# Kernel optimization log

Measured on AMD Instinct MI355X. Metric: run time of the kernel, lower is better.

Reference implementation:

```python
import jax, jax.numpy as jnp
import numpy as np

N_NODES = 20000
N_EDGES = 320000
N_GRAPHS = 200
N_LAYERS = 2
TOWERS = 5
F_IN = 75        # divide_input=False -> each tower sees the full 75-dim input
F_OUT = 15       # out_channels // towers = 75 // 5
EDGE_DIM = 50
POST_IN = (4 * 3 + 1) * F_IN  # 4 aggregators * 3 scalers + self = 975
EPS_STD = 1e-5
EPS_BN = 1e-5


def setup_inputs() -> dict:
    key = jax.random.key(0)
    ks = jax.random.split(key, 16)
    x_idx = jax.random.randint(ks[0], (N_NODES,), 0, 10000)
    edge_index = jax.random.randint(ks[1], (2, N_EDGES), 0, N_NODES)
    edge_attr_idx = jax.random.randint(ks[2], (N_EDGES,), 0, 100)
    batch_idx = jnp.sort(jax.random.randint(ks[3], (N_NODES,), 0, N_GRAPHS))

    def g(k, shp, fan):
        return jax.random.normal(k, shp, jnp.float32) * np.float32(1.0 / np.sqrt(fan))

    inp = dict(
        x_idx=x_idx, edge_index=edge_index, edge_attr_idx=edge_attr_idx, batch_idx=batch_idx,
        node_emb=g(ks[4], (10000, F_IN), 1.0),
        edge_emb=g(ks[5], (100, EDGE_DIM), 1.0),
        W_edge=g(ks[6], (N_LAYERS, EDGE_DIM, F_IN), EDGE_DIM),
        b_edge=jnp.zeros((N_LAYERS, F_IN), jnp.float32),
        W_pre=g(ks[7], (N_LAYERS, TOWERS, 3 * F_IN, F_IN), 3 * F_IN),
        b_pre=jnp.zeros((N_LAYERS, TOWERS, F_IN), jnp.float32),
        W_post=g(ks[8], (N_LAYERS, TOWERS, POST_IN, F_OUT), POST_IN),
        b_post=jnp.zeros((N_LAYERS, TOWERS, F_OUT), jnp.float32),
        W_lin=g(ks[9], (N_LAYERS, F_IN, F_IN), F_IN),
        b_lin=jnp.zeros((N_LAYERS, F_IN), jnp.float32),
        bn_gamma=jnp.ones((N_LAYERS, F_IN), jnp.float32),
        bn_beta=jnp.zeros((N_LAYERS, F_IN), jnp.float32),
        W1=g(ks[10], (75, 50), 75), b1=jnp.zeros((50,), jnp.float32),
        W2=g(ks[11], (50, 25), 50), b2=jnp.zeros((25,), jnp.float32),
        W3=g(ks[12], (25, 1), 25), b3=jnp.zeros((1,), jnp.float32),
    )
    return inp


def reference(x_idx, edge_index, edge_attr_idx, batch_idx,
              node_emb, edge_emb, W_edge, b_edge, W_pre, b_pre,
              W_post, b_post, W_lin, b_lin, bn_gamma, bn_beta,
              W1, b1, W2, b2, W3, b3):
    src, dst = edge_index[0], edge_index[1]  # flow source_to_target: aggregate at dst
    x = node_emb[x_idx]                      # [N, 75]
    e_raw = edge_emb[edge_attr_idx]          # [E, 50]

    # in-degree based scalers (PNA); avg log-degree from this graph's degree histogram
    deg = jax.ops.segment_sum(jnp.ones((N_EDGES,), jnp.float32), dst, num_segments=N_NODES)
    avg_log = jnp.mean(jnp.log(deg + 1.0))
    deg_c = jnp.maximum(deg, 1.0)
    amp = (jnp.log(deg_c + 1.0) / avg_log)[:, None, None]
    att = (avg_log / jnp.log(deg_c + 1.0))[:, None, None]
    has_in = (deg > 0.0)[:, None, None]
    inv_deg = (1.0 / deg_c)[:, None, None]

    for l in range(N_LAYERS):
        # edge encoder (shared across towers)
        e = e_raw @ W_edge[l] + b_edge[l]                            # [E, 75]
        # message: since divide_input=False all towers see the same concat input
        h = jnp.concatenate([x[dst], x[src], e], axis=-1)            # [E, 225]
        m = jnp.einsum('ec,tcf->etf', h, W_pre[l]) + b_pre[l]        # [E, T, 75]
        # multi-aggregator reduction at dst
        mean = jax.ops.segment_sum(m, dst, num_segments=N_NODES) * inv_deg
        mean_sq = jax.ops.segment_sum(m * m, dst, num_segments=N_NODES) * inv_deg
        std = jnp.sqrt(jax.nn.relu(mean_sq - mean * mean) + EPS_STD)
        mn = jnp.where(has_in, jax.ops.segment_min(m, dst, num_segments=N_NODES), 0.0)
        mx = jnp.where(has_in, jax.ops.segment_max(m, dst, num_segments=N_NODES), 0.0)
        aggr = jnp.concatenate([mean, mn, mx, std], axis=-1)         # [N, T, 300]
        # degree scalers: identity, amplification, attenuation
        out = jnp.concatenate([aggr, aggr * amp, aggr * att], axis=-1)  # [N, T, 900]
        # update: concat self features, per-tower post MLP, then shared lin
        xt = jnp.broadcast_to(x[:, None, :], (N_NODES, TOWERS, F_IN))
        h2 = jnp.concatenate([xt, out], axis=-1)                     # [N, T, 975]
        y = jnp.einsum('ntc,tcf->ntf', h2, W_post[l]) + b_post[l]    # [N, T, 15]
        y = y.reshape(N_NODES, TOWERS * F_OUT) @ W_lin[l] + b_lin[l] # [N, 75]
        # BatchNorm (training-mode batch stats, biased variance) + ReLU
        mu = jnp.mean(y, axis=0)
        var = jnp.mean((y - mu) ** 2, axis=0)
        y = (y - mu) * jax.lax.rsqrt(var + EPS_BN) * bn_gamma[l] + bn_beta[l]
        x = jax.nn.relu(y)

    pooled = jax.ops.segment_sum(x, batch_idx, num_segments=N_GRAPHS)  # [G, 75]
    h = jax.nn.relu(pooled @ W1 + b1)
    h = jax.nn.relu(h @ W2 + b2)
    return h @ W3 + b3                                               # [G, 1]
```

## Files before the change

### kernel.cpp

```cpp
#include <hip/hip_runtime.h>
#include <hip/hip_bf16.h>
#include <math.h>

#define NN 20000
#define NE 320000
#define NG 200
#define FI 75
#define NT 5
#define FO 15
#define CH 375
#define PI 975

typedef __attribute__((ext_vector_type(8))) short v8s;
typedef __attribute__((ext_vector_type(4))) float v4f;

__device__ __forceinline__ unsigned short f2bfu(float v) {
  __hip_bfloat16 h = __float2bfloat16(v);
  return *reinterpret_cast<unsigned short*>(&h);
}
__device__ __forceinline__ float uif(unsigned u) { return __uint_as_float(u); }

__global__ __launch_bounds__(256) void k_mega1(
    const int* __restrict__ xidx, const float* __restrict__ emb, float* __restrict__ x,
    const int* __restrict__ dstp, int* __restrict__ deg,
    const float* __restrict__ eemb, const float* __restrict__ W_edge,
    const float* __restrict__ b_edge, float* __restrict__ te,
    const float* __restrict__ W_pre, float* __restrict__ WAs,
    const float* __restrict__ W_post, float* __restrict__ V,
    const float* __restrict__ b_post, const float* __restrict__ W_lin,
    const float* __restrict__ b_lin, float* __restrict__ bc) {
  __shared__ float S[FI * 16];
  int b = blockIdx.x, tid = threadIdx.x;
  if (b < 5860) {
    int i = b * 256 + tid;
    if (i < NN * FI) {
      int n = i / FI, f = i - n * FI;
      x[i] = emb[xidx[n] * FI + f];
    }
  } else if (b < 7110) {
    int e = (b - 5860) * 256 + tid;
    if (e < NE) atomicAdd(&deg[dstp[e]], 1);
  } else if (b < 7310) {
    int la = b - 7110;
    int l = la / 100, a = la - l * 100;
    int f = tid;
    if (f < FI) {
      float acc = b_edge[l * FI + f];
      for (int j = 0; j < 50; ++j)
        acc = fmaf(eemb[a * 50 + j], W_edge[(l * 50 + j) * FI + f], acc);
      te[la * FI + f] = acc;
    }
  } else if (b < 7530) {
    int i = (b - 7310) * 256 + tid;
    if (i < 2 * FI * CH) {
      int c = i % CH;
      int k = (i / CH) % FI;
      int l = i / (CH * FI);
      int t = c / FI, f = c - t * FI;
      WAs[i] = W_pre[((size_t)(l * NT + t) * 225 + FI + k) * FI + f];
    }
  } else if (b < 7560) {
    int bid = b - 7530;
    int g = bid % 3;
    int lt = bid / 3;
    for (int idx = tid; idx < FI * 16; idx += 256) {
      int q = idx >> 4, f = idx & 15;
      float v = 0.f;
      if (f < FO) {
        const float* wb = W_post + (size_t)lt * PI * FO;
        int rowb = FI + g * 300 + q;
        v = wb[rowb * FO + f] + wb[(rowb + FI) * FO + f] + wb[(rowb + 2 * FI) * FO + f];
      }
      S[idx] = v;
    }
    __syncthreads();
    for (int idx = tid; idx < FI * 16; idx += 256) {
      int j = idx >> 4, f = idx & 15;
      float acc = 0.f;
      const float* wr = W_pre + ((size_t)lt * 225 + j) * FI;
      for (int q = 0; q < FI; ++q) acc = fmaf(wr[q], S[q * 16 + f], acc);
      V[((size_t)bid * FI + j) * 16 + f] = acc;
    }
  } else {
    int l = b - 7560;
    int g = tid;
    if (g < FI) {
      float acc = b_lin[l * FI + g];
      for (int j = 0; j < FI; ++j)
        acc = fmaf(b_post[l * FI + j], W_lin[(l * FI + j) * FI + g], acc);
      bc[l * 76 + g] = acc;
    }
  }
}

__global__ __launch_bounds__(1024) void k_mega2(
    const int* __restrict__ deg, int* __restrict__ off, int* __restrict__ cur,
    float* __restrict__ avglog,
    const float* __restrict__ te, const float* __restrict__ W_pre,
    const float* __restrict__ b_pre, unsigned short* __restrict__ tm,
    const float* __restrict__ W_post, const float* __restrict__ V,
    unsigned short* __restrict__ Bp,
    const float* __restrict__ WAs, unsigned short* __restrict__ Bxs,
    const float* __restrict__ W_lin, unsigned short* __restrict__ Blin) {
  __shared__ float red[1024];
  int b = blockIdx.x, t = threadIdx.x;
  if (b == 0) {
    int* wsum = (int*)red;
    int base = t * 20;
    int loc[20];
    int s = 0;
#pragma unroll
    for (int j = 0; j < 20; ++j) {
      int i = base + j;
      int v = (i < NN) ? deg[i] : 0;
      loc[j] = s;
      s += v;
    }
    int lane = t & 63, w = t >> 6;
    int inc = s;
    for (int o = 1; o < 64; o <<= 1) {
      int u = __shfl_up(inc, o, 64);
      if (lane >= o) inc += u;
    }
    if (lane == 63) wsum[w] = inc;
    __syncthreads();
    if (t == 0) {
      int a = 0;
#pragma unroll
      for (int k = 0; k < 16; ++k) { int v = wsum[k]; wsum[k] = a; a += v; }
    }
    __syncthreads();
    int tex = wsum[w] + inc - s;
#pragma unroll
    for (int j = 0; j < 20; ++j) {
      int i = base + j;
      if (i < NN) { int e = tex + loc[j]; off[i] = e; cur[i] = e; }
    }
    if (t == 1023) off[NN] = tex + s;
  } else if (b == 1) {
    float s = 0.f;
    for (int i = t; i < NN; i += 1024) s += logf((float)deg[i] + 1.f);
    red[t] = s;
    __syncthreads();
    for (int o = 512; o > 0; o >>= 1) {
      if (t < o) red[t] += red[t + o];
      __syncthreads();
    }
    if (t == 0) avglog[0] = red[0] / (float)NN;
  } else if (b < 77) {
    int idx = (b - 2) * 1024 + t;
    if (idx < 76800) {
      int la = idx / 384, c = idx - la * 384;
      int l = la / 100;
      float acc = 0.f;
      if (c < CH) {
        int tt = c / FI, f = c - tt * FI;
        acc = b_pre[(l * NT + tt) * FI + f];
        const float* ter = te + la * FI;
        for (int k = 0; k < FI; ++k)
          acc = fmaf(ter[k], W_pre[((size_t)(l * NT + tt) * 225 + 150 + k) * FI + f], acc);
      }
      tm[(size_t)la * 384 + c] = f2bfu(acc);
    }
  } else if (b < 302) {
    int i = (b - 77) * 1024 + t;
    if (i < 230400) {
      int j = i & 7;
      int lane = (i >> 3) & 63;
      int rem = i >> 9;
      int kb = rem % 15; rem /= 15;
      int g = rem % 3; rem /= 3;
      int tt = rem % 5;
      int l = rem / 5;
      int k = kb * 32 + (lane >> 4) * 8 + j;
      int f = lane & 15;
      float w = 0.f;
      if (f < FO) {
        int lt = l * NT + tt;
        if (k < 300) {
          int a = k / 75, ch = k - a * 75;
          w = W_post[((size_t)lt * PI + FI + g * 300 + a * 75 + ch) * FO + f];
        } else if (k >= 320 && k < 395) {
          w = V[(((size_t)(lt * 3 + g)) * FI + (k - 320)) * 16 + f];
        } else if (k >= 395 && k < 470 && g == 0) {
          w = W_post[((size_t)lt * PI + (k - 395)) * FO + f];
        }
      }
      Bp[i] = f2bfu(w);
    }
  } else if (b < 374) {
    int i = (b - 302) * 1024 + t;
    if (i < 73728) {
      int j = i & 7;
      int lane = (i >> 3) & 63;
      int rem = i >> 9;
      int nt = rem % 24; rem /= 24;
      int kb = rem % 3;
      int l = rem / 3;
      int k = kb * 32 + (lane >> 4) * 8 + j;
      int n = nt * 16 + (lane & 15);
      float w = 0.f;
      if (k < FI && n < CH) w = WAs[(size_t)l * FI * CH + k * CH + n];
      Bxs[i] = f2bfu(w);
    }
  } else {
    int i = (b - 374) * 1024 + t;
    if (i < 15360) {
      int j = i & 7;
      int lane = (i >> 3) & 63;
      int rem = i >> 9;
      int nt = rem % 5; rem /= 5;
      int kb = rem % 3;
      int l = rem / 3;
      int k = kb * 32 + (lane >> 4) * 8 + j;
      int f = nt * 16 + (lane & 15);
      float w = 0.f;
      if (k < FI && f < FI) w = W_lin[(size_t)l * FI * FI + k * FI + f];
      Blin[i] = f2bfu(w);
    }
  }
}

__global__ __launch_bounds__(256) void k_mega3(
    const int* __restrict__ srcp, const int* __restrict__ dstp,
    const int* __restrict__ attr, int* __restrict__ cur, int2* __restrict__ csr,
    const int* __restrict__ deg, const float* __restrict__ avglog,
    float* __restrict__ amp, float* __restrict__ att, float* __restrict__ inv) {
  int b = blockIdx.x, t = threadIdx.x;
  if (b < 1250) {
    int e = b * 256 + t;
    if (e < NE) {
      int pos = atomicAdd(&cur[dstp[e]], 1);
      csr[pos] = make_int2(srcp[e], attr[e]);
    }
  } else {
    int i = (b - 1250) * 256 + t;
    if (i < NN) {
      float dc = fmaxf((float)deg[i], 1.f);
      float ld = logf(dc + 1.f);
      float av = avglog[0];
      amp[i] = ld / av;
      att[i] = av / ld;
      inv[i] = 1.f / dc;
    }
  }
}

__global__ __launch_bounds__(256) void k_gemm_xs(const float* __restrict__ x,
                                                 const unsigned short* __restrict__ BxsL,
                                                 unsigned short* __restrict__ xsb,
                                                 const int* __restrict__ deg,
                                                 unsigned short* __restrict__ xh,
                                                 float* __restrict__ bnsum) {
  int tid = threadIdx.x;
  if (blockIdx.y == 1) {
    if (blockIdx.x == 0 && tid < 150) bnsum[tid] = 0.f;
    for (int i = blockIdx.x * 256 + tid; i < NN * 160; i += 625 * 256) {
      int r = i / 160, k = i - r * 160;
      float v = 0.f;
      if (k < FI) v = x[(size_t)r * FI + k] * ((deg[r] > 0) ? 1.f : 0.f);
      else if (k < 150) v = x[(size_t)r * FI + k - FI];
      xh[i] = f2bfu(v);
    }
    return;
  }
  __shared__ unsigned short As[32 * 104];
  __shared__ unsigned short Os[32 * 384];
  int m0 = blockIdx.x * 32;
  for (int i = tid; i < 32 * 104; i += 256) {
    int r = i / 104, k = i - r * 104;
    As[i] = (k < FI) ? f2bfu(x[(size_t)(m0 + r) * FI + k]) : 0;
  }
  __syncthreads();
  int lane = tid & 63, w = tid >> 6;
  int m16 = lane & 15, quad = lane >> 4;
  v4f acc0[6], acc1[6];
#pragma unroll
  for (int nt = 0; nt < 6; ++nt) {
    acc0[nt] = {0.f, 0.f, 0.f, 0.f};
    acc1[nt] = {0.f, 0.f, 0.f, 0.f};
  }
  const unsigned short* arow0 = As + m16 * 104 + quad * 8;
  const unsigned short* arow1 = As + (16 + m16) * 104 + quad * 8;
#pragma unroll
  for (int kb = 0; kb < 3; ++kb) {
    v8s a0 = *(const v8s*)(arow0 + kb * 32);
    v8s a1 = *(const v8s*)(arow1 + kb * 32);
#pragma unroll
    for (int nt = 0; nt < 6; ++nt) {
      v8s bf = *(const v8s*)(BxsL + ((size_t)(kb * 24 + w * 6 + nt) * 64 + lane) * 8);
      acc0[nt] = __builtin_amdgcn_mfma_f32_16x16x32_bf16(a0, bf, acc0[nt], 0, 0, 0);
      acc1[nt] = __builtin_amdgcn_mfma_f32_16x16x32_bf16(a1, bf, acc1[nt], 0, 0, 0);
    }
  }
#pragma unroll
  for (int nt = 0; nt < 6; ++nt) {
    int col = w * 96 + nt * 16 + m16;
#pragma unroll
    for (int r = 0; r < 4; ++r) {
      Os[(quad * 4 + r) * 384 + col] = f2bfu(acc0[nt][r]);
      Os[(16 + quad * 4 + r) * 384 + col] = f2bfu(acc1[nt][r]);
    }
  }
  __syncthreads();
  uint4* dst = (uint4*)(xsb + (size_t)m0 * 384);
  const uint4* src = (const uint4*)Os;
  for (int i = tid; i < 1536; i += 256) dst[i] = src[i];
}

__global__ __launch_bounds__(192) void k_aggregate(int n0, int cn,
    const unsigned short* __restrict__ xs, const int2* __restrict__ csr,
    const int* __restrict__ off, const float* __restrict__ inv_deg,
    const unsigned short* __restrict__ tm, unsigned short* __restrict__ aggA) {
  __shared__ unsigned short sm[4 * 1600];
  int tid = threadIdx.x;
  int sub = tid / 48;
  int lane48 = tid - sub * 48;
  int rel0 = blockIdx.x * 4;
  int rel = rel0 + sub;
  for (int idx = tid; idx < 400; idx += 192) {
    int h = idx / 100, pp = idx - h * 100;
    int t = pp / 20, cc = pp - t * 20;
    sm[h * 1600 + t * 320 + 300 + cc] = 0;
  }
  if (rel < cn) {
    int n = n0 + rel;
    int c0 = lane48 * 8;
    int o0 = off[n], o1 = off[n + 1];
    float s[8], q[8], mn[8], mx[8];
#pragma unroll
    for (int j = 0; j < 8; ++j) {
      s[j] = 0.f; q[j] = 0.f; mn[j] = INFINITY; mx[j] = -INFINITY;
    }
    auto proc = [&](uint4 xv, uint4 tv) {
      unsigned xa[4] = {xv.x, xv.y, xv.z, xv.w};
      unsigned ta[4] = {tv.x, tv.y, tv.z, tv.w};
#pragma unroll
      for (int j = 0; j < 4; ++j) {
        float z0 = uif(xa[j] << 16) + uif(ta[j] << 16);
        float z1 = uif(xa[j] & 0xffff0000u) + uif(ta[j] & 0xffff0000u);
        s[2 * j] += z0; q[2 * j] = fmaf(z0, z0, q[2 * j]);
        mn[2 * j] = fminf(mn[2 * j], z0); mx[2 * j] = fmaxf(mx[2 * j], z0);
        s[2 * j + 1] += z1; q[2 * j + 1] = fmaf(z1, z1, q[2 * j + 1]);
        mn[2 * j + 1] = fminf(mn[2 * j + 1], z1); mx[2 * j + 1] = fmaxf(mx[2 * j + 1], z1);
      }
    };
    int i = o0;
    for (; i + 8 <= o1; i += 8) {
      int2 e0 = csr[i], e1 = csr[i + 1], e2 = csr[i + 2], e3 = csr[i + 3];
      int2 e4 = csr[i + 4], e5 = csr[i + 5], e6 = csr[i + 6], e7 = csr[i + 7];
      uint4 x0 = *(const uint4*)(xs + (size_t)e0.x * 384 + c0);
      uint4 t0 = *(const uint4*)(tm + (size_t)e0.y * 384 + c0);
      uint4 x1 = *(const uint4*)(xs + (size_t)e1.x * 384 + c0);
      uint4 t1 = *(const uint4*)(tm + (size_t)e1.y * 384 + c0);
      uint4 x2 = *(const uint4*)(xs + (size_t)e2.x * 384 + c0);
      uint4 t2 = *(const uint4*)(tm + (size_t)e2.y * 384 + c0);
      uint4 x3 = *(const uint4*)(xs + (size_t)e3.x * 384 + c0);
      uint4 t3 = *(const uint4*)(tm + (size_t)e3.y * 384 + c0);
      uint4 x4 = *(const uint4*)(xs + (size_t)e4.x * 384 + c0);
      uint4 t4 = *(const uint4*)(tm + (size_t)e4.y * 384 + c0);
      uint4 x5 = *(const uint4*)(xs + (size_t)e5.x * 384 + c0);
      uint4 t5 = *(const uint4*)(tm + (size_t)e5.y * 384 + c0);
      uint4 x6 = *(const uint4*)(xs + (size_t)e6.x * 384 + c0);
      uint4 t6 = *(const uint4*)(tm + (size_t)e6.y * 384 + c0);
      uint4 x7 = *(const uint4*)(xs + (size_t)e7.x * 384 + c0);
      uint4 t7 = *(const uint4*)(tm + (size_t)e7.y * 384 + c0);
      proc(x0, t0); proc(x1, t1); proc(x2, t2); proc(x3, t3);
      proc(x4, t4); proc(x5, t5); proc(x6, t6); proc(x7, t7);
    }
    for (; i + 2 <= o1; i += 2) {
      int2 e0 = csr[i], e1 = csr[i + 1];
      uint4 x0 = *(const uint4*)(xs + (size_t)e0.x * 384 + c0);
      uint4 t0 = *(const uint4*)(tm + (size_t)e0.y * 384 + c0);
      uint4 x1 = *(const uint4*)(xs + (size_t)e1.x * 384 + c0);
      uint4 t1 = *(const uint4*)(tm + (size_t)e1.y * 384 + c0);
      proc(x0, t0); proc(x1, t1);
    }
    if (i < o1) {
      int2 e0 = csr[i];
      uint4 x0 = *(const uint4*)(xs + (size_t)e0.x * 384 + c0);
      uint4 t0 = *(const uint4*)(tm + (size_t)e0.y * 384 + c0);
      proc(x0, t0);
    }
    float inv = inv_deg[n];
    bool empty = (o1 == o0);
    unsigned short* srow = sm + sub * 1600;
#pragma unroll
    for (int j = 0; j < 8; ++j) {
      int c = c0 + j;
      if (c < CH) {
        float me = s[j] * inv;
        float sd = sqrtf(fmaxf(q[j] * inv - me * me, 0.f) + 1e-5f);
        float mnv = empty ? 0.f : mn[j];
        float mxv = empty ? 0.f : mx[j];
        int t = c / 75, ch = c - t * 75;
        unsigned short* bb = srow + t * 320;
        bb[ch] = f2bfu(me);
        bb[75 + ch] = f2bfu(mnv);
        bb[150 + ch] = f2bfu(mxv);
        bb[225 + ch] = f2bfu(sd);
      }
    }
  }
  __syncthreads();
  int nrow = cn - rel0;
  if (nrow > 4) nrow = 4;
  if (nrow > 0) {
    int nu4 = nrow * 200;
    uint4* dst = (uint4*)(aggA + (size_t)rel0 * 1600);
    const uint4* src = (const uint4*)sm;
    for (int idx = tid; idx < nu4; idx += 192) dst[idx] = src[idx];
  }
}

__global__ __launch_bounds__(256) void k_post2(int n0, int nend,
    const unsigned short* __restrict__ aggA, const unsigned short* __restrict__ xh,
    const unsigned short* __restrict__ Bp, const float* __restrict__ amp,
    const float* __restrict__ att, const unsigned short* __restrict__ BlinL,
    const float* __restrict__ bcL, float* __restrict__ yout,
    float* __restrict__ bnsum) {
  __shared__ unsigned short zs[64 * 96];
  __shared__ float ysum[FI], ysq[FI];
  int tid = threadIdx.x;
  if (tid < FI) { ysum[tid] = 0.f; ysq[tid] = 0.f; }
  for (int i = tid; i < 64 * 21; i += 256) {
    int r = i / 21, k = 75 + i - r * 21;
    zs[r * 96 + k] = 0;
  }
  int lane = tid & 63, wv = tid >> 6;
  int m16 = lane & 15, quad = lane >> 4;
  int relA = blockIdx.x * 64 + wv * 16 + m16;
  const unsigned short* arow = aggA + (size_t)relA * 1600 + quad * 8;
  const unsigned short* xrow = xh + (size_t)(n0 + relA) * 160 + quad * 8;
  for (int t = 0; t < NT; ++t) {
    const unsigned short* bp = Bp + ((size_t)t * 3 * 15 * 64) * 8 + lane * 8;
    v4f a0 = {0.f, 0.f, 0.f, 0.f}, a1 = a0, a2 = a0;
#pragma unroll
    for (int kb = 0; kb < 15; ++kb) {
      v8s av = *(const v8s*)((kb < 10) ? (arow + t * 320 + kb * 32)
                                       : (xrow + (kb - 10) * 32));
      const unsigned short* bb = bp + (size_t)kb * 512;
      v8s b0 = *(const v8s*)(bb);
      v8s b1 = *(const v8s*)(bb + 15 * 512);
      v8s b2 = *(const v8s*)(bb + 30 * 512);
      a0 = __builtin_amdgcn_mfma_f32_16x16x32_bf16(av, b0, a0, 0, 0, 0);
      a1 = __builtin_amdgcn_mfma_f32_16x16x32_bf16(av, b1, a1, 0, 0, 0);
      a2 = __builtin_amdgcn_mfma_f32_16x16x32_bf16(av, b2, a2, 0, 0, 0);
    }
    int f = m16;
    if (f < FO) {
      int relZ = wv * 16 + quad * 4;
#pragma unroll
      for (int r = 0; r < 4; ++r) {
        int nd = n0 + blockIdx.x * 64 + relZ + r;
        int ndc = (nd < NN) ? nd : (NN - 1);
        float zz = a0[r] + amp[ndc] * a1[r] + att[ndc] * a2[r];
        zs[(relZ + r) * 96 + t * FO + f] = f2bfu(zz);
      }
    }
  }
  __syncthreads();
  const unsigned short* zrow = zs + (wv * 16 + m16) * 96 + quad * 8;
  v4f acc2[5];
#pragma unroll
  for (int nt = 0; nt < 5; ++nt) acc2[nt] = {0.f, 0.f, 0.f, 0.f};
#pragma unroll
  for (int kb = 0; kb < 3; ++kb) {
    v8s av = *(const v8s*)(zrow + kb * 32);
#pragma unroll
    for (int nt = 0; nt < 5; ++nt) {
      v8s bl = *(const v8s*)(BlinL + ((size_t)(kb * 5 + nt) * 64 + lane) * 8);
      acc2[nt] = __builtin_amdgcn_mfma_f32_16x16x32_bf16(av, bl, acc2[nt], 0, 0, 0);
    }
  }
  int nb = n0 + blockIdx.x * 64 + wv * 16 + quad * 4;
#pragma unroll
  for (int nt = 0; nt < 5; ++nt) {
    int f = nt * 16 + m16;
    if (f < FI) {
      float bcf = bcL[f];
#pragma unroll
      for (int r = 0; r < 4; ++r) {
        int n = nb + r;
        if (n < nend) {
          float v = acc2[nt][r] + bcf;
          yout[(size_t)n * FI + f] = v;
          atomicAdd(&ysum[f], v);
          atomicAdd(&ysq[f], v * v);
        }
      }
    }
  }
  __syncthreads();
  if (tid < FI) {
    atomicAdd(&bnsum[tid], ysum[tid]);
    atomicAdd(&bnsum[FI + tid], ysq[tid]);
  }
}

__global__ __launch_bounds__(256) void k_bnfinapply(const float* __restrict__ y,
    const float* __restrict__ bnsum, const float* __restrict__ gamL,
    const float* __restrict__ betL, float* __restrict__ xo,
    const int* __restrict__ batch, float* __restrict__ pooled, int dopool) {
  __shared__ float sc[150];
  int tid = threadIdx.x;
  if (tid < FI) {
    float mu = bnsum[tid] / (float)NN;
    float var = bnsum[FI + tid] / (float)NN - mu * mu;
    float scl = gamL[tid] * rsqrtf(var + 1e-5f);
    sc[tid] = scl;
    sc[FI + tid] = betL[tid] - mu * scl;
  }
  if (!dopool) {
    for (int i = blockIdx.x * 256 + tid; i < NG * FI; i += gridDim.x * 256)
      pooled[i] = 0.f;
  }
  __syncthreads();
  int stride = gridDim.x * 256;
  for (int i = blockIdx.x * 256 + tid; i < NN * FI; i += stride) {
    int n = i / FI, f = i - n * FI;
    float v = fmaxf(fmaf(y[i], sc[f], sc[FI + f]), 0.f);
    xo[i] = v;
    if (dopool) atomicAdd(&pooled[batch[n] * FI + f], v);
  }
}

__global__ void k_head(const float* __restrict__ pooled, const float* __restrict__ W1,
                       const float* __restrict__ b1, const float* __restrict__ W2,
                       const float* __restrict__ b2, const float* __restrict__ W3,
                       const float* __restrict__ b3, float* __restrict__ out) {
  __shared__ float p[FI], h1[50], h2[25];
  int g = blockIdx.x, t = threadIdx.x;
  for (int i = t; i < FI; i += 64) p[i] = pooled[g * FI + i];
  __syncthreads();
  if (t < 50) {
    float a = b1[t];
    for (int j = 0; j < FI; ++j) a = fmaf(p[j], W1[j * 50 + t], a);
    h1[t] = fmaxf(a, 0.f);
  }
  __syncthreads();
  if (t < 25) {
    float a = b2[t];
    for (int j = 0; j < 50; ++j) a = fmaf(h1[j], W2[j * 25 + t], a);
    h2[t] = fmaxf(a, 0.f);
  }
  __syncthreads();
  if (t == 0) {
    float a = b3[0];
    for (int j = 0; j < 25; ++j) a = fmaf(h2[j], W3[j], a);
    out[g] = a;
  }
}

extern "C" void kernel_launch(void* const* d_in, const int* in_sizes, int n_in,
                              void* d_out, int out_size, void* d_ws, size_t ws_size,
                              hipStream_t stream) {
  const int* x_idx = (const int*)d_in[0];
  const int* eidx  = (const int*)d_in[1];
  const int* srcp  = eidx;
  const int* dstp  = eidx + NE;
  const int* eattr = (const int*)d_in[2];
  const int* batch = (const int*)d_in[3];
  const float* node_emb = (const float*)d_in[4];
  const float* edge_emb = (const float*)d_in[5];
  const float* W_edge = (const float*)d_in[6];
  const float* b_edge = (const float*)d_in[7];
  const float* W_pre  = (const float*)d_in[8];
  const float* b_pre  = (const float*)d_in[9];
  const float* W_post = (const float*)d_in[10];
  const float* b_post = (const float*)d_in[11];
  const float* W_lin  = (const float*)d_in[12];
  const float* b_lin  = (const float*)d_in[13];
  const float* gam = (const float*)d_in[14];
  const float* bet = (const float*)d_in[15];
  const float* W1 = (const float*)d_in[16];
  const float* b1 = (const float*)d_in[17];
  const float* W2 = (const float*)d_in[18];
  const float* b2 = (const float*)d_in[19];
  const float* W3 = (const float*)d_in[20];
  const float* b3 = (const float*)d_in[21];

  char* p = (char*)d_ws;
  auto alloc = [&](size_t b) -> char* {
    char* r = p;
    p += (b + 255) & ~(size_t)255;
    return r;
  };
  float* x_a   = (float*)alloc((size_t)NN * FI * 4);
  float* x_b   = (float*)alloc((size_t)NN * FI * 4);
  unsigned short* xs_bf = (unsigned short*)alloc((size_t)NN * 384 * 2);
  float* z     = (float*)alloc((size_t)NN * FI * 4);
  unsigned short* xh = (unsigned short*)alloc((size_t)(NN + 64) * 160 * 2);
  float* te    = (float*)alloc(2 * 100 * FI * 4);
  unsigned short* tm_bf = (unsigned short*)alloc((size_t)2 * 100 * 384 * 2);
  float* WAs   = (float*)alloc((size_t)2 * FI * CH * 4);
  float* V     = (float*)alloc((size_t)2 * NT * 3 * FI * 16 * 4);
  unsigned short* Bpk = (unsigned short*)alloc((size_t)230400 * 2);
  unsigned short* Bxs = (unsigned short*)alloc((size_t)73728 * 2);
  unsigned short* Blin = (unsigned short*)alloc((size_t)15360 * 2);
  float* bc    = (float*)alloc(2 * 76 * 4);
  float* ampv  = (float*)alloc((size_t)NN * 4);
  float* attv  = (float*)alloc((size_t)NN * 4);
  float* invv  = (float*)alloc((size_t)NN * 4);
  float* avglog = (float*)alloc(256);
  float* bnsum = (float*)alloc(2 * FI * 4);
  float* pooled = (float*)alloc((size_t)NG * FI * 4);
  int* deg = (int*)alloc((size_t)NN * 4);
  int* off = (int*)alloc((size_t)(NN + 1) * 4);
  int* cur = (int*)alloc((size_t)NN * 4);
  int2* csr = (int2*)alloc((size_t)NE * 8);
  size_t used = (size_t)(p - (char*)d_ws);
  int chunkN = NN;
  while (chunkN > 2500 &&
         used + (size_t)((chunkN + 63) & ~63) * 1600 * 2 + (1 << 20) > ws_size)
    chunkN >>= 1;
  int rows = (chunkN + 63) & ~63;
  unsigned short* aggA = (unsigned short*)alloc((size_t)rows * 1600 * 2);

  hipMemsetAsync(deg, 0, (size_t)NN * 4, stream);

  k_mega1<<<7562, 256, 0, stream>>>(x_idx, node_emb, x_a, dstp, deg,
                                    edge_emb, W_edge, b_edge, te,
                                    W_pre, WAs, W_post, V,
                                    b_post, W_lin, b_lin, bc);
  k_mega2<<<389, 1024, 0, stream>>>(deg, off, cur, avglog,
                                    te, W_pre, b_pre, tm_bf, W_post, V, Bpk,
                                    WAs, Bxs, W_lin, Blin);
  k_mega3<<<1329, 256, 0, stream>>>(srcp, dstp, eattr, cur, csr,
                                    deg, avglog, ampv, attv, invv);

  for (int l = 0; l < 2; ++l) {
    const float* xin = (l == 0) ? x_a : x_b;
    float* xout = (l == 0) ? x_b : x_a;
    k_gemm_xs<<<dim3(625, 2), 256, 0, stream>>>(xin, Bxs + (size_t)l * 36864,
                                                xs_bf, deg, xh, bnsum);
    for (int n0 = 0; n0 < NN; n0 += chunkN) {
      int cn = (NN - n0 < chunkN) ? (NN - n0) : chunkN;
      k_aggregate<<<(cn + 3) / 4, 192, 0, stream>>>(n0, cn, xs_bf, csr, off, invv,
                                                    tm_bf + (size_t)l * 100 * 384, aggA);
      k_post2<<<(cn + 63) / 64, 256, 0, stream>>>(
          n0, n0 + cn, aggA, xh, Bpk + (size_t)l * 115200, ampv, attv,
          Blin + (size_t)l * 7680, bc + l * 76, z, bnsum);
    }
    k_bnfinapply<<<1250, 256, 0, stream>>>(z, bnsum, gam + l * FI, bet + l * FI,
                                           xout, batch, pooled, (l == 1) ? 1 : 0);
  }

  k_head<<<NG, 64, 0, stream>>>(pooled, W1, b1, W2, b2, W3, b3, (float*)d_out);
}
```

Measured before the change: 465.2 us.

## Remap post-MLP kernel to one wave per tower over 16-node blocks

k_post2 now processes 16 nodes per block with 5 waves. Each wave computes one tower's post GEMM, then one 16-column slice of the shared lin GEMM. Previously each of 4 waves did all 5 towers serially for its own 16 nodes. This gives more blocks and less serial work per wave, with smaller LDS use. The trade-off is that B-matrix tiles are re-read by 4x more blocks, and the xh rows are loaded redundantly by every wave.

```diff
diff --git a/kernel.cpp b/kernel.cpp
--- a/kernel.cpp
+++ b/kernel.cpp
@@ -413,81 +413,70 @@
   }
 }
 
-__global__ __launch_bounds__(256) void k_post2(int n0, int nend,
+__global__ __launch_bounds__(320) void k_post2(int n0, int nend,
     const unsigned short* __restrict__ aggA, const unsigned short* __restrict__ xh,
     const unsigned short* __restrict__ Bp, const float* __restrict__ amp,
     const float* __restrict__ att, const unsigned short* __restrict__ BlinL,
     const float* __restrict__ bcL, float* __restrict__ yout,
     float* __restrict__ bnsum) {
-  __shared__ unsigned short zs[64 * 96];
+  __shared__ unsigned short zs[16 * 96];
   __shared__ float ysum[FI], ysq[FI];
   int tid = threadIdx.x;
+  int lane = tid & 63, wv = tid >> 6;
+  int m16 = lane & 15, quad = lane >> 4;
   if (tid < FI) { ysum[tid] = 0.f; ysq[tid] = 0.f; }
-  for (int i = tid; i < 64 * 21; i += 256) {
+  for (int i = tid; i < 16 * 21; i += 320) {
     int r = i / 21, k = 75 + i - r * 21;
     zs[r * 96 + k] = 0;
   }
-  int lane = tid & 63, wv = tid >> 6;
-  int m16 = lane & 15, quad = lane >> 4;
-  int relA = blockIdx.x * 64 + wv * 16 + m16;
-  const unsigned short* arow = aggA + (size_t)relA * 1600 + quad * 8;
+  int relA = blockIdx.x * 16 + m16;
+  const unsigned short* arow = aggA + (size_t)relA * 1600 + wv * 320 + quad * 8;
   const unsigned short* xrow = xh + (size_t)(n0 + relA) * 160 + quad * 8;
-  for (int t = 0; t < NT; ++t) {
-    const unsigned short* bp = Bp + ((size_t)t * 3 * 15 * 64) * 8 + lane * 8;
-    v4f a0 = {0.f, 0.f, 0.f, 0.f}, a1 = a0, a2 = a0;
-#pragma unroll
-    for (int kb = 0; kb < 15; ++kb) {
-      v8s av = *(const v8s*)((kb < 10) ? (arow + t * 320 + kb * 32)
-                                       : (xrow + (kb - 10) * 32));
-      const unsigned short* bb = bp + (size_t)kb * 512;
-      v8s b0 = *(const v8s*)(bb);
-      v8s b1 = *(const v8s*)(bb + 15 * 512);
-      v8s b2 = *(const v8s*)(bb + 30 * 512);
-      a0 = __builtin_amdgcn_mfma_f32_16x16x32_bf16(av, b0, a0, 0, 0, 0);
-      a1 = __builtin_amdgcn_mfma_f32_16x16x32_bf16(av, b1, a1, 0, 0, 0);
-      a2 = __builtin_amdgcn_mfma_f32_16x16x32_bf16(av, b2, a2, 0, 0, 0);
-    }
-    int f = m16;
-    if (f < FO) {
-      int relZ = wv * 16 + quad * 4;
-#pragma unroll
-      for (int r = 0; r < 4; ++r) {
-        int nd = n0 + blockIdx.x * 64 + relZ + r;
-        int ndc = (nd < NN) ? nd : (NN - 1);
-        float zz = a0[r] + amp[ndc] * a1[r] + att[ndc] * a2[r];
-        zs[(relZ + r) * 96 + t * FO + f] = f2bfu(zz);
-      }
-    }
-  }
-  __syncthreads();
-  const unsigned short* zrow = zs + (wv * 16 + m16) * 96 + quad * 8;
-  v4f acc2[5];
-#pragma unroll
-  for (int nt = 0; nt < 5; ++nt) acc2[nt] = {0.f, 0.f, 0.f, 0.f};
+  const unsigned short* bp = Bp + ((size_t)wv * 3 * 15 * 64) * 8 + lane * 8;
+  v4f a0 = {0.f, 0.f, 0.f, 0.f}, a1 = a0, a2 = a0;
+#pragma unroll
+  for (int kb = 0; kb < 15; ++kb) {
+    v8s av = *(const v8s*)((kb < 10) ? (arow + kb * 32) : (xrow + (kb - 10) * 32));
+    const unsigned short* bb = bp + (size_t)kb * 512;
+    v8s b0 = *(const v8s*)(bb);
+    v8s b1 = *(const v8s*)(bb + 15 * 512);
+    v8s b2 = *(const v8s*)(bb + 30 * 512);
+    a0 = __builtin_amdgcn_mfma_f32_16x16x32_bf16(av, b0, a0, 0, 0, 0);
+    a1 = __builtin_amdgcn_mfma_f32_16x16x32_bf16(av, b1, a1, 0, 0, 0);
+    a2 = __builtin_amdgcn_mfma_f32_16x16x32_bf16(av, b2, a2, 0, 0, 0);
+  }
+  int f = m16;
+  if (f < FO) {
+    int relZ = quad * 4;
+#pragma unroll
+    for (int r = 0; r < 4; ++r) {
+      int nd = n0 + blockIdx.x * 16 + relZ + r;
+      int ndc = (nd < NN) ? nd : (NN - 1);
+      float zz = a0[r] + amp[ndc] * a1[r] + att[ndc] * a2[r];
+      zs[(relZ + r) * 96 + wv * FO + f] = f2bfu(zz);
+    }
+  }
+  __syncthreads();
+  const unsigned short* zrow = zs + m16 * 96 + quad * 8;
+  v4f acc2 = {0.f, 0.f, 0.f, 0.f};
 #pragma unroll
   for (int kb = 0; kb < 3; ++kb) {
     v8s av = *(const v8s*)(zrow + kb * 32);
-#pragma unroll
-    for (int nt = 0; nt < 5; ++nt) {
-      v8s bl = *(const v8s*)(BlinL + ((size_t)(kb * 5 + nt) * 64 + lane) * 8);
-      acc2[nt] = __builtin_amdgcn_mfma_f32_16x16x32_bf16(av, bl, acc2[nt], 0, 0, 0);
-    }
-  }
-  int nb = n0 + blockIdx.x * 64 + wv * 16 + quad * 4;
-#pragma unroll
-  for (int nt = 0; nt < 5; ++nt) {
-    int f = nt * 16 + m16;
-    if (f < FI) {
-      float bcf = bcL[f];
-#pragma unroll
-      for (int r = 0; r < 4; ++r) {
-        int n = nb + r;
-        if (n < nend) {
-          float v = acc2[nt][r] + bcf;
-          yout[(size_t)n * FI + f] = v;
-          atomicAdd(&ysum[f], v);
-          atomicAdd(&ysq[f], v * v);
-        }
+    v8s bl = *(const v8s*)(BlinL + ((size_t)(kb * 5 + wv) * 64 + lane) * 8);
+    acc2 = __builtin_amdgcn_mfma_f32_16x16x32_bf16(av, bl, acc2, 0, 0, 0);
+  }
+  int fcol = wv * 16 + m16;
+  int nb = n0 + blockIdx.x * 16 + quad * 4;
+  if (fcol < FI) {
+    float bcf = bcL[fcol];
+#pragma unroll
+    for (int r = 0; r < 4; ++r) {
+      int n = nb + r;
+      if (n < nend) {
+        float v = acc2[r] + bcf;
+        yout[(size_t)n * FI + fcol] = v;
+        atomicAdd(&ysum[fcol], v);
+        atomicAdd(&ysq[fcol], v * v);
       }
     }
   }
@@ -638,7 +627,7 @@
       int cn = (NN - n0 < chunkN) ? (NN - n0) : chunkN;
       k_aggregate<<<(cn + 3) / 4, 192, 0, stream>>>(n0, cn, xs_bf, csr, off, invv,
                                                     tm_bf + (size_t)l * 100 * 384, aggA);
-      k_post2<<<(cn + 63) / 64, 256, 0, stream>>>(
+      k_post2<<<(cn + 15) / 16, 320, 0, stream>>>(
           n0, n0 + cn, aggA, xh, Bpk + (size_t)l * 115200, ampv, attv,
           Blin + (size_t)l * 7680, bc + l * 76, z, bnsum);
     }
```

Result: slower. 476.2 us (+2.4%).
